# Optimization experiments

Measured on AMD Instinct MI355X. Metric: run time of the kernel, lower is better.

The kernel has to match this reference:

```python
import jax, jax.numpy as jnp
import numpy as np

S = 197      # 'attention_heads' arg, acts as sequence length
D = 768      # embedding_dim
H = 4 * D    # MLP hidden
B = 64
EPS = 1e-5
SCALE = 1.0 / S ** (-0.5)  # faithful to source: equals sqrt(S)


def _ln(x, w, b):
    # LayerNorm over the last two dims (S, D), elementwise affine (S, D)
    mu = jnp.mean(x, axis=(-2, -1), keepdims=True)
    var = jnp.var(x, axis=(-2, -1), keepdims=True)
    return (x - mu) * jax.lax.rsqrt(var + EPS) * w + b


def setup_inputs() -> dict:
    key = jax.random.key(0)
    ks = jax.random.split(key, 16)
    s = 0.02
    return {
        "x": jax.random.normal(ks[0], (B, S, D), jnp.float32),
        "norm1_w": jnp.ones((S, D), jnp.float32),
        "norm1_b": jnp.zeros((S, D), jnp.float32),
        "Wq": jax.random.normal(ks[1], (D, D), jnp.float32) * s,
        "bq": jnp.zeros((D,), jnp.float32),
        "Wk": jax.random.normal(ks[2], (D, D), jnp.float32) * s,
        "bk": jnp.zeros((D,), jnp.float32),
        "Wv": jax.random.normal(ks[3], (D, D), jnp.float32) * s,
        "bv": jnp.zeros((D,), jnp.float32),
        "norm2_w": jnp.ones((S, D), jnp.float32),
        "norm2_b": jnp.zeros((S, D), jnp.float32),
        "W1": jax.random.normal(ks[4], (D, H), jnp.float32) * s,
        "b1": jnp.zeros((H,), jnp.float32),
        "W2": jax.random.normal(ks[5], (H, D), jnp.float32) * s,
        "b2": jnp.zeros((D,), jnp.float32),
    }


def reference(x, norm1_w, norm1_b, Wq, bq, Wk, bk, Wv, bv,
              norm2_w, norm2_b, W1, b1, W2, b2):
    # --- attention block ---
    h = _ln(x, norm1_w, norm1_b)                     # (B, S, D)
    q = jnp.einsum('bsd,de->bse', h, Wq) + bq
    k = jnp.einsum('bsd,de->bse', h, Wk) + bk
    v = jnp.einsum('bsd,de->bse', h, Wv) + bv
    scores = jnp.einsum('bsd,btd->bst', q, k) * SCALE  # (B, S, S)
    attn = jnp.einsum('bst,btd->bsd', jax.nn.softmax(scores, axis=-1), v)
    x = attn + x
    # --- MLP block ---
    h2 = _ln(x, norm2_w, norm2_b)
    hid = jax.nn.gelu(jnp.einsum('bsd,dh->bsh', h2, W1) + b1, approximate=False)
    mlp = jax.nn.gelu(jnp.einsum('bsh,hd->bsd', hid, W2) + b2, approximate=False)
    return mlp + x
```

## Files before the change

### kernel.cpp

```cpp
#include <hip/hip_runtime.h>
#include <math.h>


#define S_LEN 197
#define DIM   768
#define HDIM  3072
#define BATCH 64
#define NT    (BATCH * S_LEN)
#define NTP   12672
#define SD    (S_LEN * DIM)
#define SROWS 208
#define SCOLS 224
#define PROWS 256

typedef __attribute__((ext_vector_type(4))) float  f32x4;
typedef __attribute__((ext_vector_type(8))) short  short8v;
typedef __attribute__((ext_vector_type(4))) short  short4v;
typedef __attribute__((ext_vector_type(4))) unsigned short ushort4v;

__device__ __forceinline__ ushort f2bf(float f) {
  union { float f; unsigned u; } a; a.f = f;
  unsigned u = a.u;
  u += 0x7FFFu + ((u >> 16) & 1u);
  return (ushort)(u >> 16);
}
__device__ __forceinline__ float b2f(ushort h) {
  union { unsigned u; float f; } a; a.u = ((unsigned)h) << 16;
  return a.f;
}
__device__ __forceinline__ float gelu_f(float x) {
  float x3 = x * x * x;
  float y2 = 1.5957691216057308f * (x + 0.044715f * x3);
  float e  = __expf(y2);
  float t  = 1.0f - 2.0f / (e + 1.0f);
  return 0.5f * x * (1.0f + t);
}
__device__ __forceinline__ void gload16(const void* g, void* l) {
  __builtin_amdgcn_global_load_lds(
      (const __attribute__((address_space(1))) void*)g,
      (__attribute__((address_space(3))) void*)l, 16, 0, 0);
}

template<bool SPLIT>
__global__ __launch_bounds__(256) void transp_k(const float* __restrict__ W,
                                                int K, int N,
                                                ushort* __restrict__ Thi,
                                                ushort* __restrict__ Tlo) {
  __shared__ float tile[32][33];
  const int nb = blockIdx.x * 32, kb = blockIdx.y * 32;
  const int tx = threadIdx.x, ty = threadIdx.y;
#pragma unroll
  for (int i = 0; i < 4; ++i)
    tile[ty + i * 8][tx] = W[(size_t)(kb + ty + i * 8) * N + nb + tx];
  __syncthreads();
#pragma unroll
  for (int i = 0; i < 4; ++i) {
    float v = tile[tx][ty + i * 8];
    size_t o = (size_t)(nb + ty + i * 8) * K + kb + tx;
    ushort h = f2bf(v);
    Thi[o] = h;
    if (SPLIT) Tlo[o] = f2bf(v - b2f(h));
  }
}

#define LN_CH 4
__global__ __launch_bounds__(256) void ln_part_k(const float* __restrict__ x,
                                                 float* __restrict__ pbuf) {
  const int c = blockIdx.x, b = blockIdx.y;
  const float4* xv = (const float4*)(x + (size_t)b * SD);
  const int per = (SD / 4) / LN_CH;
  float sum = 0.f, sq = 0.f;
  for (int i = c * per + threadIdx.x; i < (c + 1) * per; i += 256) {
    float4 v = xv[i];
    sum += (v.x + v.y) + (v.z + v.w);
    sq  += (v.x * v.x + v.y * v.y) + (v.z * v.z + v.w * v.w);
  }
#pragma unroll
  for (int o = 32; o > 0; o >>= 1) {
    sum += __shfl_xor(sum, o); sq += __shfl_xor(sq, o);
  }
  __shared__ float s1[4], s2[4];
  if ((threadIdx.x & 63) == 0) { s1[threadIdx.x >> 6] = sum; s2[threadIdx.x >> 6] = sq; }
  __syncthreads();
  if (threadIdx.x == 0) {
    pbuf[(b * LN_CH + c) * 2]     = s1[0] + s1[1] + s1[2] + s1[3];
    pbuf[(b * LN_CH + c) * 2 + 1] = s2[0] + s2[1] + s2[2] + s2[3];
  }
}

__global__ __launch_bounds__(64) void ln_fin_k(const float* __restrict__ pbuf,
                                               float* __restrict__ stats) {
  const int b = threadIdx.x;
  float S = 0.f, Q = 0.f;
#pragma unroll
  for (int c = 0; c < LN_CH; ++c) {
    S += pbuf[(b * LN_CH + c) * 2];
    Q += pbuf[(b * LN_CH + c) * 2 + 1];
  }
  const float mu = S / (float)SD;
  const float var = Q / (float)SD - mu * mu;
  stats[b * 2] = mu;
  stats[b * 2 + 1] = 1.0f / sqrtf(var + 1e-5f);
}

template<bool SPLIT>
__global__ __launch_bounds__(256) void ln_apply_k(const float* __restrict__ x,
                                                  const float* __restrict__ w,
                                                  const float* __restrict__ bb,
                                                  const float* __restrict__ stats,
                                                  ushort* __restrict__ oHi,
                                                  ushort* __restrict__ oLo) {
  const int b = blockIdx.y;
  const int i = blockIdx.x * 256 + threadIdx.x;
  if (i >= SD / 4) return;
  const float mu = stats[b * 2], rs = stats[b * 2 + 1];
  float4 v  = ((const float4*)(x + (size_t)b * SD))[i];
  float4 W4 = ((const float4*)w)[i];
  float4 B4 = ((const float4*)bb)[i];
  float h0 = (v.x - mu) * rs * W4.x + B4.x;
  float h1 = (v.y - mu) * rs * W4.y + B4.y;
  float h2 = (v.z - mu) * rs * W4.z + B4.z;
  float h3 = (v.w - mu) * rs * W4.w + B4.w;
  ushort4v hh;
  hh[0] = f2bf(h0); hh[1] = f2bf(h1); hh[2] = f2bf(h2); hh[3] = f2bf(h3);
  ((ushort4v*)(oHi + (size_t)b * SD))[i] = hh;
  if (SPLIT) {
    ushort4v ll;
    ll[0] = f2bf(h0 - b2f(hh[0]));
    ll[1] = f2bf(h1 - b2f(hh[1]));
    ll[2] = f2bf(h2 - b2f(hh[2]));
    ll[3] = f2bf(h3 - b2f(hh[3]));
    ((ushort4v*)(oLo + (size_t)b * SD))[i] = ll;
  }
}

__global__ __launch_bounds__(64) void softmax_k(const float* __restrict__ scores,
                                                ushort* __restrict__ P) {
  const int s = blockIdx.x, b = blockIdx.y;
  const int lane = threadIdx.x;
  const float* row = scores + ((size_t)b * SROWS + s) * SCOLS;
  float v[4];
  float m = -1e30f;
#pragma unroll
  for (int t = 0; t < 4; ++t) {
    int c = lane + t * 64;
    v[t] = (c < S_LEN) ? row[c] : -1e30f;
    m = fmaxf(m, v[t]);
  }
#pragma unroll
  for (int off = 32; off > 0; off >>= 1) m = fmaxf(m, __shfl_xor(m, off));
  float sum = 0.f;
#pragma unroll
  for (int t = 0; t < 4; ++t) {
    int c = lane + t * 64;
    v[t] = (c < S_LEN) ? expf(v[t] - m) : 0.f;
    sum += v[t];
  }
#pragma unroll
  for (int off = 32; off > 0; off >>= 1) sum += __shfl_xor(sum, off);
  const float inv = 1.0f / sum;
  ushort* prow = P + ((size_t)b * PROWS + s) * SCOLS;
#pragma unroll
  for (int t = 0; t < 4; ++t) {
    int c = lane + t * 64;
    if (c < SCOLS) prow[c] = f2bf(v[t] * inv);
  }
}

#define GBM 128
#define GBN 128

enum { EPI_QK = 0, EPI_V, EPI_SCORE, EPI_PV, EPI_GELU, EPI_OUT };

struct GemmArgs {
  const ushort* Ahi; const ushort* Alo; size_t sAb; int lda;
  const ushort* Bhi; const ushort* Blo; size_t sBb; int ldb;
  int K; int Mv; int Nv;
  const float* bias;
  const float* resid; size_t sRb; int ldr;
  float scale;
  float* outF; size_t sOb; int ldo;
  ushort* outHi; ushort* outLo;
};

template<int BK>
__device__ __forceinline__ short8v frag_ld(const ushort* tile, int row, int cb) {
  constexpr int SMASK = (BK * 2) / 16 - 1;
  const char* base = (const char*)tile + row * (BK * 2);
  const int xr = (row & SMASK) << 4;
  const int c1 = cb + 32;
  union U { short8v v8; struct P4 { short4v a, b; } p4; } f;
  f.p4.a = *(const short4v*)(base + ((( cb & ~15) ^ xr) | (cb & 15)));
  f.p4.b = *(const short4v*)(base + (((c1 & ~15) ^ xr) | (c1 & 15)));
  return f.v8;
}

__device__ __forceinline__ short8v load_frag(const ushort* p) {
  union U { short8v v8; struct P4 { short4v a, b; } p4; } f;
  f.p4.a = *(const short4v*)(p);
  f.p4.b = *(const short4v*)(p + 16);
  return f.v8;
}

template<int NPROD, bool TRANSB, int EPI, int BK>
__global__ __launch_bounds__(256) void gemm_k(GemmArgs g) {
  constexpr int KSH2 = (BK == 64) ? 7 : 6;
  constexpr int SMASK = (BK * 2) / 16 - 1;
  constexpr int ASZ  = GBM * BK;
  constexpr int BSTR = TRANSB ? 44 : BK;
  constexpr int BSZ  = GBN * BSTR;
  constexpr int BUFSZ = (NPROD == 3) ? (2 * ASZ + 2 * BSZ) : (ASZ + BSZ);
  __shared__ __align__(16) ushort sm[TRANSB ? (ASZ + BSZ) : 2 * BUFSZ];

  const int tid  = threadIdx.x;
  const int lane = tid & 63;
  const int wid  = tid >> 6;
  const int r    = lane & 15;
  const int gg   = lane >> 4;
  const int wrow = wid >> 1;
  const int wcol = wid & 1;

  const int gx = gridDim.x, gy = gridDim.y;
  const int nwg = gx * gy;
  const int orig = blockIdx.x + gx * blockIdx.y;
  const int qq = nwg >> 3, rr = nwg & 7;
  const int xcd = orig & 7, idx = orig >> 3;
  const int wg = (xcd < rr ? xcd * (qq + 1) : rr * (qq + 1) + (xcd - rr) * qq) + idx;
  const int nbase = (wg % gx) * GBN;
  const int mbase = (wg / gx) * GBM;
  const int b     = blockIdx.z;

  const ushort* Ahi = g.Ahi + (size_t)b * g.sAb;
  const ushort* Bhi = g.Bhi + (size_t)b * g.sBb;
  const ushort* Alo = (NPROD == 3) ? (g.Alo + (size_t)b * g.sAb) : (const ushort*)nullptr;
  const ushort* Blo = (NPROD == 3) ? (g.Blo + (size_t)b * g.sBb) : (const ushort*)nullptr;

  f32x4 acc[4][4];
#pragma unroll
  for (int i = 0; i < 4; ++i)
#pragma unroll
    for (int j = 0; j < 4; ++j) {
      acc[i][j][0] = 0.f; acc[i][j][1] = 0.f; acc[i][j][2] = 0.f; acc[i][j][3] = 0.f;
    }

  const int wvb = wid << 10;

  auto STAGE = [&](int kk, ushort* base) {
    ushort* dA  = base;
    ushort* dB  = base + ASZ;
    ushort* dAl = base + ASZ + BSZ;
    ushort* dBl = base + 2 * ASZ + BSZ;
#pragma unroll
    for (int rd = 0; rd < BK / 16; ++rd) {
      const int boff = rd * 4096 + tid * 16;
      const int row  = boff >> KSH2;
      const int slot = (boff >> 4) & SMASK;
      const int scol = ((slot ^ (row & SMASK)) << 3);
      const size_t gaoff = (size_t)(mbase + row) * g.lda + (kk + scol);
      gload16(Ahi + gaoff, (char*)dA + rd * 4096 + wvb);
      if (NPROD == 3)
        gload16(Alo + gaoff, (char*)dAl + rd * 4096 + wvb);
      const size_t gboff = (size_t)(nbase + row) * g.ldb + (kk + scol);
      gload16(Bhi + gboff, (char*)dB + rd * 4096 + wvb);
      if (NPROD == 3)
        gload16(Blo + gboff, (char*)dBl + rd * 4096 + wvb);
    }
  };

  auto COMPUTE = [&](const ushort* base) {
    const ushort* cA  = base;
    const ushort* cB  = base + ASZ;
    const ushort* cAl = base + ASZ + BSZ;
    const ushort* cBl = base + 2 * ASZ + BSZ;
#pragma unroll
    for (int kb = 0; kb < BK / 32; ++kb) {
      const int cbk = kb * 64 + gg * 8;
      short8v aH[4], bH[4], aL[4], bL[4];
#pragma unroll
      for (int i = 0; i < 4; ++i) {
        const int arow = wrow * 64 + i * 16 + r;
        aH[i] = frag_ld<BK>(cA, arow, cbk);
        if (NPROD == 3) aL[i] = frag_ld<BK>(cAl, arow, cbk);
      }
#pragma unroll
      for (int j = 0; j < 4; ++j) {
        const int brow = wcol * 64 + j * 16 + r;
        bH[j] = frag_ld<BK>(cB, brow, cbk);
        if (NPROD == 3) bL[j] = frag_ld<BK>(cBl, brow, cbk);
      }
#pragma unroll
      for (int i = 0; i < 4; ++i)
#pragma unroll
        for (int j = 0; j < 4; ++j) {
          acc[i][j] = __builtin_amdgcn_mfma_f32_16x16x32_bf16(aH[i], bH[j], acc[i][j], 0, 0, 0);
          if (NPROD == 3) {
            acc[i][j] = __builtin_amdgcn_mfma_f32_16x16x32_bf16(aH[i], bL[j], acc[i][j], 0, 0, 0);
            acc[i][j] = __builtin_amdgcn_mfma_f32_16x16x32_bf16(aL[i], bH[j], acc[i][j], 0, 0, 0);
          }
        }
    }
  };

  if (!TRANSB) {
    STAGE(0, sm);
    __syncthreads();
    const int nst = g.K / BK;
    for (int t = 0; t < nst; ++t) {
      ushort* cur = sm + (t & 1) * BUFSZ;
      ushort* nxt = sm + ((t & 1) ^ 1) * BUFSZ;
      if (t + 1 < nst) STAGE((t + 1) * BK, nxt);
      COMPUTE(cur);
      if (t + 1 < nst) __syncthreads();
    }
  } else {
    ushort* sAhi = sm;
    ushort* sBhi = sm + ASZ;
    for (int kk = 0; kk < g.K; kk += BK) {
      __syncthreads();
#pragma unroll
      for (int rd = 0; rd < BK / 16; ++rd) {
        const int boff = rd * 4096 + tid * 16;
        const int row  = boff >> KSH2;
        const int slot = (boff >> 4) & SMASK;
        const int scol = ((slot ^ (row & SMASK)) << 3);
        const size_t gaoff = (size_t)(mbase + row) * g.lda + (kk + scol);
        gload16(Ahi + gaoff, (char*)sAhi + rd * 4096 + wvb);
      }
#pragma unroll
      for (int rd = 0; rd < (BK * 128) / 2048; ++rd) {
        const int lin = tid * 8 + rd * 2048;
        const int kr = lin >> 7, nc = lin & 127;
        union { short8v v; ushort u[8]; } t;
        t.v = *(const short8v*)(Bhi + (size_t)(kk + kr) * g.ldb + (nbase + nc));
#pragma unroll
        for (int e = 0; e < 8; ++e)
          sBhi[(nc + e) * BSTR + kr] = t.u[e];
      }
      __syncthreads();
#pragma unroll
      for (int kb = 0; kb < BK / 32; ++kb) {
        const int cbk = kb * 64 + gg * 8;
        short8v aH[4], bH[4];
#pragma unroll
        for (int i = 0; i < 4; ++i)
          aH[i] = frag_ld<BK>(sAhi, wrow * 64 + i * 16 + r, cbk);
#pragma unroll
        for (int j = 0; j < 4; ++j)
          bH[j] = load_frag(sBhi + (wcol * 64 + j * 16 + r) * BSTR + kb * 32 + gg * 4);
#pragma unroll
        for (int i = 0; i < 4; ++i)
#pragma unroll
          for (int j = 0; j < 4; ++j)
            acc[i][j] = __builtin_amdgcn_mfma_f32_16x16x32_bf16(aH[i], bH[j], acc[i][j], 0, 0, 0);
      }
    }
  }

#pragma unroll
  for (int i = 0; i < 4; ++i)
#pragma unroll
    for (int j = 0; j < 4; ++j)
#pragma unroll
      for (int e = 0; e < 4; ++e) {
        const int row = mbase + wrow * 64 + i * 16 + gg * 4 + e;
        const int col = nbase + wcol * 64 + j * 16 + r;
        float val = acc[i][j][e];
        if (EPI == EPI_QK) {
          val += g.bias[col];
          ushort hi = f2bf(val);
          ushort lo = f2bf(val - b2f(hi));
          size_t o = (size_t)row * g.ldo + col;
          g.outHi[o] = hi; g.outLo[o] = lo;
        } else if (EPI == EPI_V) {
          val += g.bias[col];
          g.outHi[(size_t)row * g.ldo + col] = f2bf(val);
        } else if (EPI == EPI_SCORE) {
          if (row < g.Mv && col < g.Nv)
            (g.outF + (size_t)b * g.sOb)[(size_t)row * g.ldo + col] = val * g.scale;
        } else if (EPI == EPI_PV) {
          if (row < g.Mv) {
            val += (g.resid + (size_t)b * g.sRb)[(size_t)row * g.ldr + col];
            (g.outF + (size_t)b * g.sOb)[(size_t)row * g.ldo + col] = val;
          }
        } else if (EPI == EPI_GELU) {
          val = gelu_f(val + g.bias[col]);
          g.outHi[(size_t)row * g.ldo + col] = f2bf(val);
        } else {
          if (row < g.Mv) {
            val = gelu_f(val + g.bias[col]);
            val += g.resid[(size_t)row * g.ldr + col];
            g.outF[(size_t)row * g.ldo + col] = val;
          }
        }
      }
}

extern "C" void kernel_launch(void* const* d_in, const int* in_sizes, int n_in,
                              void* d_out, int out_size, void* d_ws, size_t ws_size,
                              hipStream_t stream) {
  const float* x   = (const float*)d_in[0];
  const float* n1w = (const float*)d_in[1];
  const float* n1b = (const float*)d_in[2];
  const float* Wq  = (const float*)d_in[3];
  const float* bq  = (const float*)d_in[4];
  const float* Wk  = (const float*)d_in[5];
  const float* bk  = (const float*)d_in[6];
  const float* Wv  = (const float*)d_in[7];
  const float* bv  = (const float*)d_in[8];
  const float* n2w = (const float*)d_in[9];
  const float* n2b = (const float*)d_in[10];
  const float* W1  = (const float*)d_in[11];
  const float* b1  = (const float*)d_in[12];
  const float* W2  = (const float*)d_in[13];
  const float* b2  = (const float*)d_in[14];
  float* out = (float*)d_out;

  char* ws = (char*)d_ws;
  size_t off = 0;
  auto alloc = [&](size_t bytes) -> char* {
    char* p = ws + off;
    off += (bytes + 255) & ~(size_t)255;
    return p;
  };
  const size_t szDD  = (size_t)DIM * DIM * 2;
  const size_t szDH  = (size_t)DIM * HDIM * 2;
  const size_t szAct = (size_t)NTP * DIM * 2;

  ushort* wqtH = (ushort*)alloc(szDD);
  ushort* wqtL = (ushort*)alloc(szDD);
  ushort* wktH = (ushort*)alloc(szDD);
  ushort* wktL = (ushort*)alloc(szDD);
  ushort* wvtH = (ushort*)alloc(szDD);
  ushort* w1tH = (ushort*)alloc(szDH);
  ushort* w2tH = (ushort*)alloc(szDH);
  ushort* hHi  = (ushort*)alloc(szAct);
  ushort* hLo  = (ushort*)alloc(szAct);
  ushort* qHi  = (ushort*)alloc(szAct);
  ushort* qLo  = (ushort*)alloc(szAct);
  ushort* kHi  = (ushort*)alloc(szAct);
  ushort* kLo  = (ushort*)alloc(szAct);
  ushort* vB   = (ushort*)alloc(szAct);
  float*  scoresWs = (float*)alloc((size_t)BATCH * SROWS * SCOLS * 4);
  ushort* pWs      = (ushort*)alloc((size_t)BATCH * PROWS * SCOLS * 2);
  float*  lnPart   = (float*)alloc((size_t)BATCH * LN_CH * 2 * 4);
  float*  lnStats  = (float*)alloc((size_t)BATCH * 2 * 4);
  if (off > ws_size) return;

  float*  x2  = (float*)hHi;
  ushort* h2  = vB;
  ushort* hid = qHi;

  const float SCALE_F = 14.035668847618199f;

  dim3 tb(32, 8);
  hipLaunchKernelGGL((transp_k<true >), dim3(DIM / 32, DIM / 32), tb, 0, stream, Wq, DIM, DIM, wqtH, wqtL);
  hipLaunchKernelGGL((transp_k<true >), dim3(DIM / 32, DIM / 32), tb, 0, stream, Wk, DIM, DIM, wktH, wktL);
  hipLaunchKernelGGL((transp_k<false>), dim3(DIM / 32, DIM / 32), tb, 0, stream, Wv, DIM, DIM, wvtH, (ushort*)nullptr);
  hipLaunchKernelGGL((transp_k<false>), dim3(HDIM / 32, DIM / 32), tb, 0, stream, W1, DIM, HDIM, w1tH, (ushort*)nullptr);
  hipLaunchKernelGGL((transp_k<false>), dim3(DIM / 32, HDIM / 32), tb, 0, stream, W2, HDIM, DIM, w2tH, (ushort*)nullptr);

  const int APPLY_BX = (SD / 4 + 255) / 256;
  hipLaunchKernelGGL(ln_part_k, dim3(LN_CH, BATCH), dim3(256), 0, stream, x, lnPart);
  hipLaunchKernelGGL(ln_fin_k, dim3(1), dim3(64), 0, stream, lnPart, lnStats);
  hipLaunchKernelGGL((ln_apply_k<true>), dim3(APPLY_BX, BATCH), dim3(256), 0, stream,
                     x, n1w, n1b, lnStats, hHi, hLo);

  GemmArgs a;
  const int BIG = 0x40000000;

  a = GemmArgs{};
  a.Ahi = hHi; a.Alo = hLo; a.sAb = 0; a.lda = DIM;
  a.Bhi = wqtH; a.Blo = wqtL; a.sBb = 0; a.ldb = DIM;
  a.K = DIM; a.Mv = BIG; a.Nv = BIG; a.bias = bq; a.scale = 1.f;
  a.outHi = qHi; a.outLo = qLo; a.ldo = DIM;
  hipLaunchKernelGGL((gemm_k<3, false, EPI_QK, 32>), dim3(DIM / GBN, NTP / GBM, 1), dim3(256), 0, stream, a);
  a.Bhi = wktH; a.Blo = wktL; a.bias = bk; a.outHi = kHi; a.outLo = kLo;
  hipLaunchKernelGGL((gemm_k<3, false, EPI_QK, 32>), dim3(DIM / GBN, NTP / GBM, 1), dim3(256), 0, stream, a);
  a = GemmArgs{};
  a.Ahi = hHi; a.sAb = 0; a.lda = DIM;
  a.Bhi = wvtH; a.sBb = 0; a.ldb = DIM;
  a.K = DIM; a.Mv = BIG; a.Nv = BIG; a.bias = bv;
  a.outHi = vB; a.ldo = DIM;
  hipLaunchKernelGGL((gemm_k<1, false, EPI_V, 64>), dim3(DIM / GBN, NTP / GBM, 1), dim3(256), 0, stream, a);

  a = GemmArgs{};
  a.Ahi = qHi; a.Alo = qLo; a.sAb = (size_t)SD; a.lda = DIM;
  a.Bhi = kHi; a.Blo = kLo; a.sBb = (size_t)SD; a.ldb = DIM;
  a.K = DIM; a.Mv = S_LEN; a.Nv = S_LEN; a.scale = SCALE_F;
  a.outF = scoresWs; a.sOb = (size_t)SROWS * SCOLS; a.ldo = SCOLS;
  hipLaunchKernelGGL((gemm_k<3, false, EPI_SCORE, 32>), dim3(2, 2, BATCH), dim3(256), 0, stream, a);

  hipLaunchKernelGGL(softmax_k, dim3(S_LEN, BATCH), dim3(64), 0, stream, scoresWs, pWs);

  a = GemmArgs{};
  a.Ahi = pWs; a.sAb = (size_t)PROWS * SCOLS; a.lda = SCOLS;
  a.Bhi = vB; a.sBb = (size_t)SD; a.ldb = DIM;
  a.K = SCOLS; a.Mv = S_LEN; a.Nv = BIG;
  a.resid = x; a.sRb = (size_t)SD; a.ldr = DIM;
  a.outF = x2; a.sOb = (size_t)SD; a.ldo = DIM;
  hipLaunchKernelGGL((gemm_k<1, true, EPI_PV, 32>), dim3(DIM / GBN, 2, BATCH), dim3(256), 0, stream, a);

  hipLaunchKernelGGL(ln_part_k, dim3(LN_CH, BATCH), dim3(256), 0, stream, x2, lnPart);
  hipLaunchKernelGGL(ln_fin_k, dim3(1), dim3(64), 0, stream, lnPart, lnStats);
  hipLaunchKernelGGL((ln_apply_k<false>), dim3(APPLY_BX, BATCH), dim3(256), 0, stream,
                     x2, n2w, n2b, lnStats, h2, (ushort*)nullptr);

  a = GemmArgs{};
  a.Ahi = h2; a.sAb = 0; a.lda = DIM;
  a.Bhi = w1tH; a.sBb = 0; a.ldb = DIM;
  a.K = DIM; a.Mv = BIG; a.Nv = BIG; a.bias = b1;
  a.outHi = hid; a.ldo = HDIM;
  hipLaunchKernelGGL((gemm_k<1, false, EPI_GELU, 64>), dim3(HDIM / GBN, NTP / GBM, 1), dim3(256), 0, stream, a);

  a = GemmArgs{};
  a.Ahi = hid; a.sAb = 0; a.lda = HDIM;
  a.Bhi = w2tH; a.sBb = 0; a.ldb = HDIM;
  a.K = HDIM; a.Mv = NT; a.Nv = BIG; a.bias = b2;
  a.resid = x2; a.sRb = 0; a.ldr = DIM;
  a.outF = out; a.sOb = 0; a.ldo = DIM;
  hipLaunchKernelGGL((gemm_k<1, false, EPI_OUT, 64>), dim3(DIM / GBN, NTP / GBM, 1), dim3(256), 0, stream, a);
}
```

Baseline: 753.3 us.

## Fuse QKV projections into one GEMM and use larger 512-thread GEMM tiles

```diff
diff --git a/kernel.cpp b/kernel.cpp
--- a/kernel.cpp
+++ b/kernel.cpp
@@ -7,8 +7,10 @@
 #define HDIM  3072
 #define BATCH 64
 #define NT    (BATCH * S_LEN)
-#define NTP   12672
+#define MP    12800
+#define QKVN  2304
 #define SD    (S_LEN * DIM)
+#define SQK   (S_LEN * QKVN)
 #define SROWS 208
 #define SCOLS 224
 #define PROWS 256
@@ -167,16 +169,13 @@
   }
 }
 
-#define GBM 128
-#define GBN 128
-
-enum { EPI_QK = 0, EPI_V, EPI_SCORE, EPI_PV, EPI_GELU, EPI_OUT };
+enum { EPI_QKV = 0, EPI_SCORE, EPI_PV, EPI_GELU, EPI_OUT };
 
 struct GemmArgs {
   const ushort* Ahi; const ushort* Alo; size_t sAb; int lda;
   const ushort* Bhi; const ushort* Blo; size_t sBb; int ldb;
   int K; int Mv; int Nv;
-  const float* bias;
+  const float* bias; const float* biasK; const float* biasV;
   const float* resid; size_t sRb; int ldr;
   float scale;
   float* outF; size_t sOb; int ldo;
@@ -202,13 +201,159 @@
   return f.v8;
 }
 
+__device__ __forceinline__ int xcd_swz(int orig, int nwg) {
+  const int qq = nwg >> 3, rr = nwg & 7;
+  const int xcd = orig & 7, idx = orig >> 3;
+  return (xcd < rr ? xcd * (qq + 1) : rr * (qq + 1) + (xcd - rr) * qq) + idx;
+}
+
+template<int NPROD, int EPI, int BK, int MR, int NR>
+__global__ __launch_bounds__(512) void gemm2_k(GemmArgs g) {
+  constexpr int WC = 4;
+  constexpr int BM = 2 * MR * 16;
+  constexpr int BN = WC * NR * 16;
+  constexpr int KSH2 = (BK == 64) ? 7 : 6;
+  constexpr int SMASK = (BK * 2) / 16 - 1;
+  constexpr int ASZ = BM * BK;
+  constexpr int BSZ = BN * BK;
+  constexpr int BUFSZ = (NPROD == 3) ? 2 * (ASZ + BSZ) : (ASZ + BSZ);
+  __shared__ __align__(16) ushort sm[2 * BUFSZ];
+
+  const int tid  = threadIdx.x;
+  const int lane = tid & 63;
+  const int wid  = tid >> 6;
+  const int r    = lane & 15;
+  const int gg   = lane >> 4;
+  const int wrow = wid >> 2;
+  const int wcol = wid & 3;
+
+  const int gx = gridDim.x, gy = gridDim.y;
+  const int wg = xcd_swz(blockIdx.x + gx * blockIdx.y, gx * gy);
+  const int nbase = (wg % gx) * BN;
+  const int mbase = (wg / gx) * BM;
+
+  const ushort* Ahi = g.Ahi;
+  const ushort* Bhi = g.Bhi;
+  const ushort* Alo = g.Alo;
+  const ushort* Blo = g.Blo;
+
+  f32x4 acc[MR][NR];
+#pragma unroll
+  for (int i = 0; i < MR; ++i)
+#pragma unroll
+    for (int j = 0; j < NR; ++j) {
+      acc[i][j][0] = 0.f; acc[i][j][1] = 0.f; acc[i][j][2] = 0.f; acc[i][j][3] = 0.f;
+    }
+
+  const int wvb = wid << 10;
+
+  auto STAGE = [&](int kk, ushort* base) {
+    ushort* dA  = base;
+    ushort* dB  = base + ASZ;
+    ushort* dAl = base + ASZ + BSZ;
+    ushort* dBl = base + 2 * ASZ + BSZ;
+#pragma unroll
+    for (int rd = 0; rd < (ASZ * 2) / 8192; ++rd) {
+      const int boff = rd * 8192 + tid * 16;
+      const int row  = boff >> KSH2;
+      const int slot = (boff >> 4) & SMASK;
+      const int scol = (slot ^ (row & SMASK)) << 3;
+      const size_t ga = (size_t)(mbase + row) * g.lda + (kk + scol);
+      gload16(Ahi + ga, (char*)dA + rd * 8192 + wvb);
+      if (NPROD == 3) gload16(Alo + ga, (char*)dAl + rd * 8192 + wvb);
+    }
+#pragma unroll
+    for (int rd = 0; rd < (BSZ * 2) / 8192; ++rd) {
+      const int boff = rd * 8192 + tid * 16;
+      const int row  = boff >> KSH2;
+      const int slot = (boff >> 4) & SMASK;
+      const int scol = (slot ^ (row & SMASK)) << 3;
+      const size_t gb = (size_t)(nbase + row) * g.ldb + (kk + scol);
+      gload16(Bhi + gb, (char*)dB + rd * 8192 + wvb);
+      if (NPROD == 3) gload16(Blo + gb, (char*)dBl + rd * 8192 + wvb);
+    }
+  };
+
+  auto COMPUTE = [&](const ushort* base) {
+    const ushort* cA  = base;
+    const ushort* cB  = base + ASZ;
+    const ushort* cAl = base + ASZ + BSZ;
+    const ushort* cBl = base + 2 * ASZ + BSZ;
+#pragma unroll
+    for (int kb = 0; kb < BK / 32; ++kb) {
+      const int cbk = kb * 64 + gg * 8;
+      short8v bH[NR], bL[NR];
+#pragma unroll
+      for (int j = 0; j < NR; ++j) {
+        const int brow = wcol * (NR * 16) + j * 16 + r;
+        bH[j] = frag_ld<BK>(cB, brow, cbk);
+        if (NPROD == 3) bL[j] = frag_ld<BK>(cBl, brow, cbk);
+      }
+#pragma unroll
+      for (int i = 0; i < MR; ++i) {
+        const int arow = wrow * (MR * 16) + i * 16 + r;
+        short8v aH = frag_ld<BK>(cA, arow, cbk);
+        short8v aL = aH;
+        if (NPROD == 3) aL = frag_ld<BK>(cAl, arow, cbk);
+#pragma unroll
+        for (int j = 0; j < NR; ++j) {
+          acc[i][j] = __builtin_amdgcn_mfma_f32_16x16x32_bf16(aH, bH[j], acc[i][j], 0, 0, 0);
+          if (NPROD == 3) {
+            acc[i][j] = __builtin_amdgcn_mfma_f32_16x16x32_bf16(aH, bL[j], acc[i][j], 0, 0, 0);
+            acc[i][j] = __builtin_amdgcn_mfma_f32_16x16x32_bf16(aL, bH[j], acc[i][j], 0, 0, 0);
+          }
+        }
+      }
+    }
+  };
+
+  STAGE(0, sm);
+  __syncthreads();
+  const int nst = g.K / BK;
+  for (int t = 0; t < nst; ++t) {
+    ushort* cur = sm + (t & 1) * BUFSZ;
+    ushort* nxt = sm + ((t & 1) ^ 1) * BUFSZ;
+    if (t + 1 < nst) STAGE((t + 1) * BK, nxt);
+    COMPUTE(cur);
+    if (t + 1 < nst) __syncthreads();
+  }
+
+#pragma unroll
+  for (int i = 0; i < MR; ++i)
+#pragma unroll
+    for (int j = 0; j < NR; ++j)
+#pragma unroll
+      for (int e = 0; e < 4; ++e) {
+        const int row = mbase + wrow * (MR * 16) + i * 16 + gg * 4 + e;
+        const int col = nbase + wcol * (NR * 16) + j * 16 + r;
+        if (row >= g.Mv) continue;
+        float val = acc[i][j][e];
+        if (EPI == EPI_QKV) {
+          const int seg = nbase / 768;
+          const float* bp = (seg == 0) ? g.bias : (seg == 1 ? g.biasK : g.biasV);
+          val += bp[col - seg * 768];
+          ushort hi = f2bf(val);
+          ushort lo = f2bf(val - b2f(hi));
+          size_t o = (size_t)row * g.ldo + col;
+          g.outHi[o] = hi; g.outLo[o] = lo;
+        } else if (EPI == EPI_GELU) {
+          val = gelu_f(val + g.bias[col]);
+          g.outHi[(size_t)row * g.ldo + col] = f2bf(val);
+        } else {
+          val = gelu_f(val + g.bias[col]);
+          val += g.resid[(size_t)row * g.ldr + col];
+          g.outF[(size_t)row * g.ldo + col] = val;
+        }
+      }
+}
+
 template<int NPROD, bool TRANSB, int EPI, int BK>
 __global__ __launch_bounds__(256) void gemm_k(GemmArgs g) {
   constexpr int KSH2 = (BK == 64) ? 7 : 6;
   constexpr int SMASK = (BK * 2) / 16 - 1;
-  constexpr int ASZ  = GBM * BK;
+  constexpr int ASZ  = 128 * BK;
   constexpr int BSTR = TRANSB ? 44 : BK;
-  constexpr int BSZ  = GBN * BSTR;
+  constexpr int BSZ  = 128 * BSTR;
   constexpr int BUFSZ = (NPROD == 3) ? (2 * ASZ + 2 * BSZ) : (ASZ + BSZ);
   __shared__ __align__(16) ushort sm[TRANSB ? (ASZ + BSZ) : 2 * BUFSZ];
 
@@ -221,13 +366,9 @@
   const int wcol = wid & 1;
 
   const int gx = gridDim.x, gy = gridDim.y;
-  const int nwg = gx * gy;
-  const int orig = blockIdx.x + gx * blockIdx.y;
-  const int qq = nwg >> 3, rr = nwg & 7;
-  const int xcd = orig & 7, idx = orig >> 3;
-  const int wg = (xcd < rr ? xcd * (qq + 1) : rr * (qq + 1) + (xcd - rr) * qq) + idx;
-  const int nbase = (wg % gx) * GBN;
-  const int mbase = (wg / gx) * GBM;
+  const int wg = xcd_swz(blockIdx.x + gx * blockIdx.y, gx * gy);
+  const int nbase = (wg % gx) * 128;
+  const int mbase = (wg / gx) * 128;
   const int b     = blockIdx.z;
 
   const ushort* Ahi = g.Ahi + (size_t)b * g.sAb;
@@ -365,31 +506,13 @@
         const int row = mbase + wrow * 64 + i * 16 + gg * 4 + e;
         const int col = nbase + wcol * 64 + j * 16 + r;
         float val = acc[i][j][e];
-        if (EPI == EPI_QK) {
-          val += g.bias[col];
-          ushort hi = f2bf(val);
-          ushort lo = f2bf(val - b2f(hi));
-          size_t o = (size_t)row * g.ldo + col;
-          g.outHi[o] = hi; g.outLo[o] = lo;
-        } else if (EPI == EPI_V) {
-          val += g.bias[col];
-          g.outHi[(size_t)row * g.ldo + col] = f2bf(val);
-        } else if (EPI == EPI_SCORE) {
+        if (EPI == EPI_SCORE) {
           if (row < g.Mv && col < g.Nv)
             (g.outF + (size_t)b * g.sOb)[(size_t)row * g.ldo + col] = val * g.scale;
         } else if (EPI == EPI_PV) {
           if (row < g.Mv) {
             val += (g.resid + (size_t)b * g.sRb)[(size_t)row * g.ldr + col];
             (g.outF + (size_t)b * g.sOb)[(size_t)row * g.ldo + col] = val;
-          }
-        } else if (EPI == EPI_GELU) {
-          val = gelu_f(val + g.bias[col]);
-          g.outHi[(size_t)row * g.ldo + col] = f2bf(val);
-        } else {
-          if (row < g.Mv) {
-            val = gelu_f(val + g.bias[col]);
-            val += g.resid[(size_t)row * g.ldr + col];
-            g.outF[(size_t)row * g.ldo + col] = val;
           }
         }
       }
@@ -422,24 +545,16 @@
     off += (bytes + 255) & ~(size_t)255;
     return p;
   };
-  const size_t szDD  = (size_t)DIM * DIM * 2;
-  const size_t szDH  = (size_t)DIM * HDIM * 2;
-  const size_t szAct = (size_t)NTP * DIM * 2;
-
-  ushort* wqtH = (ushort*)alloc(szDD);
-  ushort* wqtL = (ushort*)alloc(szDD);
-  ushort* wktH = (ushort*)alloc(szDD);
-  ushort* wktL = (ushort*)alloc(szDD);
-  ushort* wvtH = (ushort*)alloc(szDD);
-  ushort* w1tH = (ushort*)alloc(szDH);
-  ushort* w2tH = (ushort*)alloc(szDH);
-  ushort* hHi  = (ushort*)alloc(szAct);
-  ushort* hLo  = (ushort*)alloc(szAct);
-  ushort* qHi  = (ushort*)alloc(szAct);
-  ushort* qLo  = (ushort*)alloc(szAct);
-  ushort* kHi  = (ushort*)alloc(szAct);
-  ushort* kLo  = (ushort*)alloc(szAct);
-  ushort* vB   = (ushort*)alloc(szAct);
+
+  ushort* wqkvtH = (ushort*)alloc((size_t)QKVN * DIM * 2);
+  ushort* wqkvtL = (ushort*)alloc((size_t)QKVN * DIM * 2);
+  ushort* w1tH   = (ushort*)alloc((size_t)DIM * HDIM * 2);
+  ushort* w2tH   = (ushort*)alloc((size_t)DIM * HDIM * 2);
+  ushort* hHi    = (ushort*)alloc((size_t)MP * DIM * 2);
+  ushort* hLo    = (ushort*)alloc((size_t)MP * DIM * 2);
+  ushort* qkvHi  = (ushort*)alloc((size_t)MP * QKVN * 2);
+  ushort* qkvLo  = (ushort*)alloc((size_t)MP * QKVN * 2);
+  ushort* h2     = (ushort*)alloc((size_t)MP * DIM * 2);
   float*  scoresWs = (float*)alloc((size_t)BATCH * SROWS * SCOLS * 4);
   ushort* pWs      = (ushort*)alloc((size_t)BATCH * PROWS * SCOLS * 2);
   float*  lnPart   = (float*)alloc((size_t)BATCH * LN_CH * 2 * 4);
@@ -447,17 +562,21 @@
   if (off > ws_size) return;
 
   float*  x2  = (float*)hHi;
-  ushort* h2  = vB;
-  ushort* hid = qHi;
+  ushort* hid = qkvHi;
 
   const float SCALE_F = 14.035668847618199f;
 
   dim3 tb(32, 8);
-  hipLaunchKernelGGL((transp_k<true >), dim3(DIM / 32, DIM / 32), tb, 0, stream, Wq, DIM, DIM, wqtH, wqtL);
-  hipLaunchKernelGGL((transp_k<true >), dim3(DIM / 32, DIM / 32), tb, 0, stream, Wk, DIM, DIM, wktH, wktL);
-  hipLaunchKernelGGL((transp_k<false>), dim3(DIM / 32, DIM / 32), tb, 0, stream, Wv, DIM, DIM, wvtH, (ushort*)nullptr);
-  hipLaunchKernelGGL((transp_k<false>), dim3(HDIM / 32, DIM / 32), tb, 0, stream, W1, DIM, HDIM, w1tH, (ushort*)nullptr);
-  hipLaunchKernelGGL((transp_k<false>), dim3(DIM / 32, HDIM / 32), tb, 0, stream, W2, HDIM, DIM, w2tH, (ushort*)nullptr);
+  hipLaunchKernelGGL((transp_k<true >), dim3(DIM / 32, DIM / 32), tb, 0, stream,
+                     Wq, DIM, DIM, wqkvtH, wqkvtL);
+  hipLaunchKernelGGL((transp_k<true >), dim3(DIM / 32, DIM / 32), tb, 0, stream,
+                     Wk, DIM, DIM, wqkvtH + (size_t)768 * DIM, wqkvtL + (size_t)768 * DIM);
+  hipLaunchKernelGGL((transp_k<true >), dim3(DIM / 32, DIM / 32), tb, 0, stream,
+                     Wv, DIM, DIM, wqkvtH + (size_t)1536 * DIM, wqkvtL + (size_t)1536 * DIM);
+  hipLaunchKernelGGL((transp_k<false>), dim3(HDIM / 32, DIM / 32), tb, 0, stream,
+                     W1, DIM, HDIM, w1tH, (ushort*)nullptr);
+  hipLaunchKernelGGL((transp_k<false>), dim3(DIM / 32, HDIM / 32), tb, 0, stream,
+                     W2, HDIM, DIM, w2tH, (ushort*)nullptr);
 
   const int APPLY_BX = (SD / 4 + 255) / 256;
   hipLaunchKernelGGL(ln_part_k, dim3(LN_CH, BATCH), dim3(256), 0, stream, x, lnPart);
@@ -470,35 +589,31 @@
 
   a = GemmArgs{};
   a.Ahi = hHi; a.Alo = hLo; a.sAb = 0; a.lda = DIM;
-  a.Bhi = wqtH; a.Blo = wqtL; a.sBb = 0; a.ldb = DIM;
-  a.K = DIM; a.Mv = BIG; a.Nv = BIG; a.bias = bq; a.scale = 1.f;
-  a.outHi = qHi; a.outLo = qLo; a.ldo = DIM;
-  hipLaunchKernelGGL((gemm_k<3, false, EPI_QK, 32>), dim3(DIM / GBN, NTP / GBM, 1), dim3(256), 0, stream, a);
-  a.Bhi = wktH; a.Blo = wktL; a.bias = bk; a.outHi = kHi; a.outLo = kLo;
-  hipLaunchKernelGGL((gemm_k<3, false, EPI_QK, 32>), dim3(DIM / GBN, NTP / GBM, 1), dim3(256), 0, stream, a);
+  a.Bhi = wqkvtH; a.Blo = wqkvtL; a.sBb = 0; a.ldb = DIM;
+  a.K = DIM; a.Mv = NT; a.Nv = BIG;
+  a.bias = bq; a.biasK = bk; a.biasV = bv;
+  a.outHi = qkvHi; a.outLo = qkvLo; a.ldo = QKVN;
+  hipLaunchKernelGGL((gemm2_k<3, EPI_QKV, 32, 8, 2>), dim3(QKVN / 128, MP / 256, 1),
+                     dim3(512), 0, stream, a);
+
   a = GemmArgs{};
-  a.Ahi = hHi; a.sAb = 0; a.lda = DIM;
-  a.Bhi = wvtH; a.sBb = 0; a.ldb = DIM;
-  a.K = DIM; a.Mv = BIG; a.Nv = BIG; a.bias = bv;
-  a.outHi = vB; a.ldo = DIM;
-  hipLaunchKernelGGL((gemm_k<1, false, EPI_V, 64>), dim3(DIM / GBN, NTP / GBM, 1), dim3(256), 0, stream, a);
-
-  a = GemmArgs{};
-  a.Ahi = qHi; a.Alo = qLo; a.sAb = (size_t)SD; a.lda = DIM;
-  a.Bhi = kHi; a.Blo = kLo; a.sBb = (size_t)SD; a.ldb = DIM;
+  a.Ahi = qkvHi; a.Alo = qkvLo; a.sAb = (size_t)SQK; a.lda = QKVN;
+  a.Bhi = qkvHi + 768; a.Blo = qkvLo + 768; a.sBb = (size_t)SQK; a.ldb = QKVN;
   a.K = DIM; a.Mv = S_LEN; a.Nv = S_LEN; a.scale = SCALE_F;
   a.outF = scoresWs; a.sOb = (size_t)SROWS * SCOLS; a.ldo = SCOLS;
-  hipLaunchKernelGGL((gemm_k<3, false, EPI_SCORE, 32>), dim3(2, 2, BATCH), dim3(256), 0, stream, a);
+  hipLaunchKernelGGL((gemm_k<3, false, EPI_SCORE, 32>), dim3(2, 2, BATCH),
+                     dim3(256), 0, stream, a);
 
   hipLaunchKernelGGL(softmax_k, dim3(S_LEN, BATCH), dim3(64), 0, stream, scoresWs, pWs);
 
   a = GemmArgs{};
   a.Ahi = pWs; a.sAb = (size_t)PROWS * SCOLS; a.lda = SCOLS;
-  a.Bhi = vB; a.sBb = (size_t)SD; a.ldb = DIM;
+  a.Bhi = qkvHi + 1536; a.sBb = (size_t)SQK; a.ldb = QKVN;
   a.K = SCOLS; a.Mv = S_LEN; a.Nv = BIG;
   a.resid = x; a.sRb = (size_t)SD; a.ldr = DIM;
   a.outF = x2; a.sOb = (size_t)SD; a.ldo = DIM;
-  hipLaunchKernelGGL((gemm_k<1, true, EPI_PV, 32>), dim3(DIM / GBN, 2, BATCH), dim3(256), 0, stream, a);
+  hipLaunchKernelGGL((gemm_k<1, true, EPI_PV, 32>), dim3(DIM / 128, 2, BATCH),
+                     dim3(256), 0, stream, a);
 
   hipLaunchKernelGGL(ln_part_k, dim3(LN_CH, BATCH), dim3(256), 0, stream, x2, lnPart);
   hipLaunchKernelGGL(ln_fin_k, dim3(1), dim3(64), 0, stream, lnPart, lnStats);
@@ -508,9 +623,10 @@
   a = GemmArgs{};
   a.Ahi = h2; a.sAb = 0; a.lda = DIM;
   a.Bhi = w1tH; a.sBb = 0; a.ldb = DIM;
-  a.K = DIM; a.Mv = BIG; a.Nv = BIG; a.bias = b1;
+  a.K = DIM; a.Mv = NT; a.Nv = BIG; a.bias = b1;
   a.outHi = hid; a.ldo = HDIM;
-  hipLaunchKernelGGL((gemm_k<1, false, EPI_GELU, 64>), dim3(HDIM / GBN, NTP / GBM, 1), dim3(256), 0, stream, a);
+  hipLaunchKernelGGL((gemm2_k<1, EPI_GELU, 64, 8, 4>), dim3(HDIM / 256, MP / 256, 1),
+                     dim3(512), 0, stream, a);
 
   a = GemmArgs{};
   a.Ahi = hid; a.sAb = 0; a.lda = HDIM;
@@ -518,5 +634,6 @@
   a.K = HDIM; a.Mv = NT; a.Nv = BIG; a.bias = b2;
   a.resid = x2; a.sRb = 0; a.ldr = DIM;
   a.outF = out; a.sOb = 0; a.ldo = DIM;
-  hipLaunchKernelGGL((gemm_k<1, false, EPI_OUT, 64>), dim3(DIM / GBN, NTP / GBM, 1), dim3(256), 0, stream, a);
-}
+  hipLaunchKernelGGL((gemm2_k<1, EPI_OUT, 64, 8, 4>), dim3(DIM / 256, MP / 256, 1),
+                     dim3(512), 0, stream, a);
+}
```

Measured after the change: 874.3 us. +16.1%, slower.
